# Kernel optimization log

Hardware: AMD Instinct MI355X
Metric: run time of the kernel (lower is better)

Reference implementation:

```python
import jax, jax.numpy as jnp
import numpy as np

NUM_ROIS = 200  # Schaefer200: labels 1..200, 0 = background


def setup_inputs() -> dict:
    key = jax.random.key(0)
    k1, k2 = jax.random.split(key)
    B, C, D, H, W = 4, 256, 46, 55, 46
    feature_map = jax.random.normal(k1, (B, C, D, H, W), dtype=jnp.float32)
    # atlas already at the feature-map resolution (nearest resample is identity here)
    atlas = jax.random.randint(k2, (D, H, W), 0, NUM_ROIS + 1, dtype=jnp.int32)
    return {"feature_map": feature_map, "atlas": atlas}


def reference(feature_map, atlas):
    B, C, D, H, W = feature_map.shape
    N = D * H * W
    seg = atlas.reshape(N)                      # int labels in [0, NUM_ROIS]
    feats = feature_map.reshape(B, C, N)
    # single-pass segment mean keyed by atlas label (segment 0 = background)
    sums = jax.ops.segment_sum(
        jnp.transpose(feats, (2, 0, 1)),        # (N, B, C)
        seg, num_segments=NUM_ROIS + 1)         # (NUM_ROIS+1, B, C)
    counts = jax.ops.segment_sum(
        jnp.ones((N,), dtype=feature_map.dtype), seg,
        num_segments=NUM_ROIS + 1)              # (NUM_ROIS+1,)
    roi_sums = jnp.transpose(sums, (1, 0, 2))[:, 1:, :]   # (B, NUM_ROIS, C)
    roi_counts = counts[1:]                                # (NUM_ROIS,)
    valid = roi_counts > 0                                 # (NUM_ROIS,)
    denom = jnp.where(valid, roi_counts, 1.0)[None, :, None]
    roi_features = jnp.where(valid[None, :, None], roi_sums / denom, 0.0)
    roi_valid_mask = jnp.broadcast_to(valid[None, :], (B, NUM_ROIS))
    return roi_features, roi_valid_mask
```

## Files before the change

kernel.cpp:

```cpp
#include <hip/hip_runtime.h>

#define NB 4
#define NC 256
#define NN 116380
#define NVEC (NN/4)
#define NR 200
#define NL 201
#define NPLANES (NB*NC)
#define NFEAT (NB*NR*NC)
#define MROI 256
#define CHV 64
#define NCH 1818
#define NTAIL 28
#define PPB 128
#define AOFFD (PPB*64)
#define BUFD (AOFFD + 64)
#define NBUF 2

typedef __attribute__((ext_vector_type(8))) short bf16x8;
typedef __attribute__((ext_vector_type(4))) float f32x4;

union BU { uint4 u; bf16x8 v; };

__device__ __forceinline__ unsigned pkbf(float x, float y) {
    unsigned ux = __float_as_uint(x) + 0x8000u;
    unsigned uy = __float_as_uint(y) + 0x8000u;
    return __builtin_amdgcn_perm(uy, ux, 0x07060302u);
}
__device__ __forceinline__ unsigned oh2(int l0, int l1, int c) {
    return (l0 == c ? 0x3F80u : 0u) | (l1 == c ? 0x3F800000u : 0u);
}
__device__ __forceinline__ bf16x8 mkA(const int4& la, const int4& lb, int c) {
    union { unsigned u[4]; bf16x8 v; } x;
    x.u[0] = oh2(la.x, la.y, c);
    x.u[1] = oh2(la.z, la.w, c);
    x.u[2] = oh2(lb.x, lb.y, c);
    x.u[3] = oh2(lb.z, lb.w, c);
    return x.v;
}

__global__ __launch_bounds__(256) void roi_count(const int* __restrict__ atlas,
                                                 float* __restrict__ counts) {
    __shared__ float h[NL];
    const int tid = threadIdx.x;
    for (int i = tid; i < NL; i += 256) h[i] = 0.0f;
    __syncthreads();
    const int iv = blockIdx.x * 256 + tid;
    if (iv < NVEC) {
        int4 lab = ((const int4*)atlas)[iv];
        atomicAdd(&h[lab.x], 1.0f);
        atomicAdd(&h[lab.y], 1.0f);
        atomicAdd(&h[lab.z], 1.0f);
        atomicAdd(&h[lab.w], 1.0f);
    }
    __syncthreads();
    for (int i = tid; i < NL; i += 256) {
        float v = h[i];
        if (i > 0 && v != 0.0f) atomicAdd(&counts[i - 1], v);
    }
}

__global__ __launch_bounds__(256, 2) void roi_accum_w(const float* __restrict__ fm,
                                                      const int* __restrict__ atlas,
                                                      float* __restrict__ partials) {
    __shared__ unsigned lds[NBUF * BUFD];
    const int tid  = threadIdx.x;
    const int wave = tid >> 6;
    const int lane = tid & 63;
    const int g    = lane >> 4;
    const int n    = lane & 15;
    const int pb   = blockIdx.y * PPB;
    const int x    = blockIdx.x;
    const int gx   = gridDim.x;

    const int base = NCH / gx, rem = NCH % gx;
    const int c0 = x * base + min(x, rem);
    const int c1 = c0 + base + (x < rem ? 1 : 0);

    f32x4 acc[4][8];
    #pragma unroll
    for (int t = 0; t < 4; ++t)
        #pragma unroll
        for (int p = 0; p < 8; ++p)
            acc[t][p] = (f32x4){0.f, 0.f, 0.f, 0.f};

    const int t0    = wave * 4;
    const int cbase = t0 * 16 + n + 1;
    const int NT    = (wave == 3) ? 1 : 4;

    auto STAGE = [&](int ch, int b) {
        #pragma unroll
        for (int j = 0; j < 8; ++j) {
            const int row  = (wave * 8 + j) * 4 + (lane >> 4);
            const int colp = (lane & 15) * 4;
            const int col  = colp ^ ((row & 7) << 2);
            const float* gp = fm + (size_t)(pb + row) * NN + ch * CHV + col;
            unsigned* lp = &lds[b * BUFD + (wave * 8 + j) * 256];
            __builtin_amdgcn_global_load_lds(
                (const __attribute__((address_space(1))) unsigned*)gp,
                (__attribute__((address_space(3))) unsigned*)lp, 16, 0, 0);
        }
        const int* ga = atlas + ch * CHV + lane;
        __builtin_amdgcn_global_load_lds(
            (const __attribute__((address_space(1))) unsigned*)ga,
            (__attribute__((address_space(3))) unsigned*)&lds[b * BUFD + AOFFD], 4, 0, 0);
    };

    auto CONSUME_KS = [&](int b, int ks) {
        const unsigned* ap = &lds[b * BUFD + AOFFD + ks * 32 + 8 * g];
        int4 la = *(const int4*)ap;
        int4 lb = *(const int4*)(ap + 4);
        bf16x8 A0 = mkA(la, lb, cbase);
        bf16x8 A1 = mkA(la, lb, cbase + 16);
        bf16x8 A2 = mkA(la, lb, cbase + 32);
        bf16x8 A3 = mkA(la, lb, cbase + 48);
        #pragma unroll
        for (int p = 0; p < 8; ++p) {
            const int row = p * 16 + n;
            const int xr  = (row & 7) << 2;
            const int cb  = ks * 32 + g * 8;
            f32x4 f0 = *(const f32x4*)&lds[b * BUFD + row * 64 + (cb ^ xr)];
            f32x4 f1 = *(const f32x4*)&lds[b * BUFD + row * 64 + ((cb + 4) ^ xr)];
            BU B;
            B.u = make_uint4(pkbf(f0[0], f0[1]), pkbf(f0[2], f0[3]),
                             pkbf(f1[0], f1[1]), pkbf(f1[2], f1[3]));
            acc[0][p] = __builtin_amdgcn_mfma_f32_16x16x32_bf16(A0, B.v, acc[0][p], 0, 0, 0);
            if (NT > 1) {
                acc[1][p] = __builtin_amdgcn_mfma_f32_16x16x32_bf16(A1, B.v, acc[1][p], 0, 0, 0);
                acc[2][p] = __builtin_amdgcn_mfma_f32_16x16x32_bf16(A2, B.v, acc[2][p], 0, 0, 0);
                acc[3][p] = __builtin_amdgcn_mfma_f32_16x16x32_bf16(A3, B.v, acc[3][p], 0, 0, 0);
            }
        }
    };

    if (c0 + 0 < c1) STAGE(c0 + 0, 0);
    if (c0 + 1 < c1) STAGE(c0 + 1, 1);

    int b = 0;
    for (int c = c0; c < c1; ++c) {
        const int ahead = min(c1, c + 2) - (c + 1);
        if (ahead >= 1) asm volatile("s_waitcnt vmcnt(9)" ::: "memory");
        else            asm volatile("s_waitcnt vmcnt(0)" ::: "memory");
        __builtin_amdgcn_s_barrier();
        __builtin_amdgcn_sched_barrier(0);
        CONSUME_KS(b, 0);
        CONSUME_KS(b, 1);
        __builtin_amdgcn_sched_barrier(0);
        __builtin_amdgcn_s_barrier();
        if (c + 2 < c1) STAGE(c + 2, b);
        b ^= 1;
    }

    if (c1 == NCH && c0 < c1) {
        const int row = tid >> 1;
        const int hh  = tid & 1;
        const int xr  = (row & 7) << 2;
        #pragma unroll
        for (int i = 0; i < 16; ++i) {
            const int cl = hh * 16 + i;
            float v = (cl < NTAIL) ? fm[(size_t)(pb + row) * NN + NCH * CHV + cl] : 0.0f;
            lds[row * 64 + (cl ^ xr)] = __float_as_uint(v);
        }
        if (tid < CHV) {
            int a = (tid < NTAIL) ? atlas[NCH * CHV + tid] : 0;
            lds[AOFFD + tid] = (unsigned)a;
        }
        __syncthreads();
        CONSUME_KS(0, 0);
    }

    float* pc = partials + (size_t)x * (MROI * NPLANES);
    const int rbase = 4 * g;
    #pragma unroll
    for (int t = 0; t < 4; ++t) {
        if (t < NT) {
            #pragma unroll
            for (int p = 0; p < 8; ++p)
                #pragma unroll
                for (int i = 0; i < 4; ++i)
                    pc[(size_t)((t0 + t) * 16 + rbase + i) * NPLANES + (pb + 16 * p + n)] = acc[t][p][i];
        }
    }
}

__global__ __launch_bounds__(256) void roi_final2(const float* __restrict__ partials,
                                                  const float* __restrict__ counts,
                                                  float* __restrict__ out,
                                                  const int kch) {
    const int j = blockIdx.x * 256 + threadIdx.x;
    if (j < NFEAT) {
        const int c = j & (NC - 1);
        const int r = (j >> 8) % NR;
        const int bb = j / (NR * NC);
        const int plane = bb * NC + c;
        float s = 0.0f;
        for (int ch = 0; ch < kch; ++ch)
            s += partials[((size_t)ch * MROI + r) * NPLANES + plane];
        const float cnt = counts[r];
        out[j] = (cnt > 0.0f) ? s / cnt : 0.0f;
    } else if (j < NFEAT + NB * NR) {
        const int r = (j - NFEAT) % NR;
        out[j] = (counts[r] > 0.0f) ? 1.0f : 0.0f;
    }
}

extern "C" void kernel_launch(void* const* d_in, const int* in_sizes, int n_in,
                              void* d_out, int out_size, void* d_ws, size_t ws_size,
                              hipStream_t stream) {
    const float* fm    = (const float*)d_in[0];
    const int*   atlas = (const int*)d_in[1];
    float*       out   = (float*)d_out;

    float* counts   = (float*)d_ws;
    float* partials = counts + 256;

    int kch = 64;
    while (kch > 16 &&
           ws_size < 1024 + (size_t)kch * MROI * NPLANES * sizeof(float))
        kch >>= 1;

    hipMemsetAsync(counts, 0, NR * sizeof(float), stream);

    roi_count<<<(NVEC + 255) / 256, 256, 0, stream>>>(atlas, counts);

    roi_accum_w<<<dim3(kch, NPLANES / PPB), 256, 0, stream>>>(fm, atlas, partials);

    const int total = NFEAT + NB * NR;
    roi_final2<<<(total + 255) / 256, 256, 0, stream>>>(partials, counts, out, kch);
}
```

Measured before the change: 150.5 us.

## Retile ROI accumulation to 64 planes by 96 voxels with three K-steps

The MFMA accumulation kernel now processes 64 feature planes per block instead of 128, with 96-voxel chunks (three K-steps of 32) instead of 64. The grid becomes 48 voxel-chunk splits by 16 plane tiles, and the launch bound allows 3 blocks per CU. Accumulator registers are halved, and the one-hot A fragments for the last wave are built only when needed. The aim is more blocks in flight and more work per barrier. The trade-off is less reuse of the one-hot label fragments across planes and different waitcnt tuning.

```diff
diff --git a/kernel.cpp b/kernel.cpp
--- a/kernel.cpp
+++ b/kernel.cpp
@@ -9,12 +9,11 @@
 #define NPLANES (NB*NC)
 #define NFEAT (NB*NR*NC)
 #define MROI 256
-#define CHV 64
-#define NCH 1818
+#define CHV 96
+#define NCH 1212
 #define NTAIL 28
-#define PPB 128
-#define AOFFD (PPB*64)
-#define BUFD (AOFFD + 64)
+#define AOFFD (64*CHV)
+#define BUFD (AOFFD + 256)
 #define NBUF 2
 
 typedef __attribute__((ext_vector_type(8))) short bf16x8;
@@ -60,16 +59,16 @@
     }
 }
 
-__global__ __launch_bounds__(256, 2) void roi_accum_w(const float* __restrict__ fm,
-                                                      const int* __restrict__ atlas,
-                                                      float* __restrict__ partials) {
+__global__ __launch_bounds__(256, 3) void roi_accum_96(const float* __restrict__ fm,
+                                                       const int* __restrict__ atlas,
+                                                       float* __restrict__ partials) {
     __shared__ unsigned lds[NBUF * BUFD];
     const int tid  = threadIdx.x;
     const int wave = tid >> 6;
     const int lane = tid & 63;
     const int g    = lane >> 4;
     const int n    = lane & 15;
-    const int pb   = blockIdx.y * PPB;
+    const int pb   = blockIdx.y * 64;
     const int x    = blockIdx.x;
     const int gx   = gridDim.x;
 
@@ -77,11 +76,11 @@
     const int c0 = x * base + min(x, rem);
     const int c1 = c0 + base + (x < rem ? 1 : 0);
 
-    f32x4 acc[4][8];
+    f32x4 acc[4][4];
     #pragma unroll
     for (int t = 0; t < 4; ++t)
         #pragma unroll
-        for (int p = 0; p < 8; ++p)
+        for (int p = 0; p < 4; ++p)
             acc[t][p] = (f32x4){0.f, 0.f, 0.f, 0.f};
 
     const int t0    = wave * 4;
@@ -90,37 +89,42 @@
 
     auto STAGE = [&](int ch, int b) {
         #pragma unroll
-        for (int j = 0; j < 8; ++j) {
-            const int row  = (wave * 8 + j) * 4 + (lane >> 4);
-            const int colp = (lane & 15) * 4;
-            const int col  = colp ^ ((row & 7) << 2);
-            const float* gp = fm + (size_t)(pb + row) * NN + ch * CHV + col;
-            unsigned* lp = &lds[b * BUFD + (wave * 8 + j) * 256];
+        for (int j = 0; j < 6; ++j) {
+            const int d    = wave * 1536 + j * 256 + lane * 4;
+            const int row  = d / CHV;
+            const int col  = d - row * CHV;
+            const int scol = col ^ ((row & 7) << 2);
+            const float* gp = fm + (size_t)(pb + row) * NN + ch * CHV + scol;
+            unsigned* lp = &lds[b * BUFD + wave * 1536 + j * 256];
             __builtin_amdgcn_global_load_lds(
                 (const __attribute__((address_space(1))) unsigned*)gp,
                 (__attribute__((address_space(3))) unsigned*)lp, 16, 0, 0);
         }
-        const int* ga = atlas + ch * CHV + lane;
-        __builtin_amdgcn_global_load_lds(
-            (const __attribute__((address_space(1))) unsigned*)ga,
-            (__attribute__((address_space(3))) unsigned*)&lds[b * BUFD + AOFFD], 4, 0, 0);
+        if (lane < 24) {
+            const int* ga = atlas + ch * CHV + lane * 4;
+            __builtin_amdgcn_global_load_lds(
+                (const __attribute__((address_space(1))) unsigned*)ga,
+                (__attribute__((address_space(3))) unsigned*)&lds[b * BUFD + AOFFD], 16, 0, 0);
+        }
     };
 
     auto CONSUME_KS = [&](int b, int ks) {
         const unsigned* ap = &lds[b * BUFD + AOFFD + ks * 32 + 8 * g];
         int4 la = *(const int4*)ap;
         int4 lb = *(const int4*)(ap + 4);
-        bf16x8 A0 = mkA(la, lb, cbase);
-        bf16x8 A1 = mkA(la, lb, cbase + 16);
-        bf16x8 A2 = mkA(la, lb, cbase + 32);
-        bf16x8 A3 = mkA(la, lb, cbase + 48);
-        #pragma unroll
-        for (int p = 0; p < 8; ++p) {
+        bf16x8 A0 = mkA(la, lb, cbase), A1, A2, A3;
+        if (NT > 1) {
+            A1 = mkA(la, lb, cbase + 16);
+            A2 = mkA(la, lb, cbase + 32);
+            A3 = mkA(la, lb, cbase + 48);
+        }
+        #pragma unroll
+        for (int p = 0; p < 4; ++p) {
             const int row = p * 16 + n;
             const int xr  = (row & 7) << 2;
             const int cb  = ks * 32 + g * 8;
-            f32x4 f0 = *(const f32x4*)&lds[b * BUFD + row * 64 + (cb ^ xr)];
-            f32x4 f1 = *(const f32x4*)&lds[b * BUFD + row * 64 + ((cb + 4) ^ xr)];
+            f32x4 f0 = *(const f32x4*)&lds[b * BUFD + row * CHV + (cb ^ xr)];
+            f32x4 f1 = *(const f32x4*)&lds[b * BUFD + row * CHV + ((cb + 4) ^ xr)];
             BU B;
             B.u = make_uint4(pkbf(f0[0], f0[1]), pkbf(f0[2], f0[3]),
                              pkbf(f1[0], f1[1]), pkbf(f1[2], f1[3]));
@@ -138,13 +142,13 @@
 
     int b = 0;
     for (int c = c0; c < c1; ++c) {
-        const int ahead = min(c1, c + 2) - (c + 1);
-        if (ahead >= 1) asm volatile("s_waitcnt vmcnt(9)" ::: "memory");
+        if (c + 1 < c1) asm volatile("s_waitcnt vmcnt(7)" ::: "memory");
         else            asm volatile("s_waitcnt vmcnt(0)" ::: "memory");
         __builtin_amdgcn_s_barrier();
         __builtin_amdgcn_sched_barrier(0);
         CONSUME_KS(b, 0);
         CONSUME_KS(b, 1);
+        CONSUME_KS(b, 2);
         __builtin_amdgcn_sched_barrier(0);
         __builtin_amdgcn_s_barrier();
         if (c + 2 < c1) STAGE(c + 2, b);
@@ -152,16 +156,15 @@
     }
 
     if (c1 == NCH && c0 < c1) {
-        const int row = tid >> 1;
-        const int hh  = tid & 1;
+        const int row = tid >> 2, scq = tid & 3;
         const int xr  = (row & 7) << 2;
         #pragma unroll
-        for (int i = 0; i < 16; ++i) {
-            const int cl = hh * 16 + i;
-            float v = (cl < NTAIL) ? fm[(size_t)(pb + row) * NN + NCH * CHV + cl] : 0.0f;
-            lds[row * 64 + (cl ^ xr)] = __float_as_uint(v);
-        }
-        if (tid < CHV) {
+        for (int i = 0; i < 8; ++i) {
+            const int cl = scq * 8 + i;
+            float v = (cl < NTAIL) ? fm[(size_t)(pb + row) * NN + (size_t)NCH * CHV + cl] : 0.0f;
+            lds[row * CHV + (cl ^ xr)] = __float_as_uint(v);
+        }
+        if (tid < 32) {
             int a = (tid < NTAIL) ? atlas[NCH * CHV + tid] : 0;
             lds[AOFFD + tid] = (unsigned)a;
         }
@@ -175,7 +178,7 @@
     for (int t = 0; t < 4; ++t) {
         if (t < NT) {
             #pragma unroll
-            for (int p = 0; p < 8; ++p)
+            for (int p = 0; p < 4; ++p)
                 #pragma unroll
                 for (int i = 0; i < 4; ++i)
                     pc[(size_t)((t0 + t) * 16 + rbase + i) * NPLANES + (pb + 16 * p + n)] = acc[t][p][i];
@@ -214,8 +217,8 @@
     float* counts   = (float*)d_ws;
     float* partials = counts + 256;
 
-    int kch = 64;
-    while (kch > 16 &&
+    int kch = 48;
+    while (kch > 12 &&
            ws_size < 1024 + (size_t)kch * MROI * NPLANES * sizeof(float))
         kch >>= 1;
 
@@ -223,7 +226,7 @@
 
     roi_count<<<(NVEC + 255) / 256, 256, 0, stream>>>(atlas, counts);
 
-    roi_accum_w<<<dim3(kch, NPLANES / PPB), 256, 0, stream>>>(fm, atlas, partials);
+    roi_accum_96<<<dim3(kch, 16), 256, 0, stream>>>(fm, atlas, partials);
 
     const int total = NFEAT + NB * NR;
     roi_final2<<<(total + 255) / 256, 256, 0, stream>>>(partials, counts, out, kch);
```

New measurement: 137.1 us. -8.9%, faster.
